# Kernel optimization log

Measured on AMD Instinct MI355X. Metric: run time of the kernel, lower is better.

The kernel has to match this reference:

```python
import jax, jax.numpy as jnp
import numpy as np

N, E, D = 50000, 512000, 128

def mish(x):
    return x * jnp.tanh(jax.nn.softplus(x))

def ln(x, g, b):
    m = jnp.mean(x, axis=-1, keepdims=True)
    v = jnp.var(x, axis=-1, keepdims=True)
    return (x - m) / jnp.sqrt(v + 1e-5) * g + b

def setup_inputs():
    key = jax.random.key(0)
    ks = jax.random.split(key, 16)
    W = lambda k, i, o: jax.random.normal(k, (i, o), jnp.float32) * 0.02
    z = jnp.zeros((D,), jnp.float32)
    o = jnp.ones((D,), jnp.float32)
    return {
        "node_feat": jax.random.normal(ks[0], (N, D), jnp.float32),
        "coord_feat": jax.random.normal(ks[1], (N, D), jnp.float32),
        "Wq": W(ks[2], D, D), "bq": z, "gq": o, "beq": z,
        "Wk": W(ks[3], D, D), "bk": z, "gk": o, "bek": z,
        "Wm1": W(ks[4], D, D), "bm1": z, "gm": o, "bem": z,
        "Wm2": W(ks[5], D, D), "bm2": z,
        "Wb1": W(ks[6], D, D), "bb1": z, "gb": o, "beb": z,
        "Wb2": W(ks[7], D, D), "bb2": z,
        "Ww1": W(ks[8], D, D), "bw1": z, "gw": o, "bew": z,
        "Ww2": W(ks[9], D, D), "bw2": z,
        "Wn1": W(ks[10], 2 * D, D), "bn1": z,
        "Wn2": W(ks[11], D, D), "bn2": z,
        "Wc1": W(ks[12], D, D), "bc1": z,
        "Wc2": W(ks[13], D, D),
        "src": jax.random.randint(ks[14], (E,), 0, N, jnp.int32),
        "dst": jax.random.randint(ks[15], (E,), 0, N, jnp.int32),
    }

def reference(node_feat, coord_feat, Wq, bq, gq, beq, Wk, bk, gk, bek,
              Wm1, bm1, gm, bem, Wm2, bm2, Wb1, bb1, gb, beb, Wb2, bb2,
              Ww1, bw1, gw, bew, Ww2, bw2, Wn1, bn1, Wn2, bn2, Wc1, bc1, Wc2,
              src, dst):
    # linear_q / linear_k on coord features: Linear -> LayerNorm -> Mish
    q = mish(ln(coord_feat @ Wq + bq, gq, beq))   # [N, D]
    k = mish(ln(coord_feat @ Wk + bk, gk, bek))   # [N, D]
    # u_sub_v('q','k'): per-edge q[src] - k[dst]
    rel = q[src] - k[dst]                          # [E, D]
    radial = jnp.sum(rel * rel, axis=-1, keepdims=True)  # [E, 1]
    rel = rel / jnp.sqrt(radial + 1e-8)
    # relative position encodings from dst coord features
    xd = coord_feat[dst]                           # [E, D]
    pem = mish(ln(xd @ Wm1 + bm1, gm, bem)) @ Wm2 + bm2
    peb = mish(ln(xd @ Wb1 + bb1, gb, beb)) @ Wb2 + bb2
    rel = rel * pem + peb
    # weight_encoding MLP
    w = mish(ln(rel @ Ww1 + bw1, gw, bew)) @ Ww2 + bw2  # [E, D]
    # dgl.softmax_edges over a single graph: softmax across the edge axis
    w = jax.nn.softmax(w, axis=0)
    # update_all(copy_e, sum): scatter-add edge weights to destination nodes
    h_neigh = jax.ops.segment_sum(w, dst, num_segments=N)  # [N, D]
    h = mish(jnp.concatenate([node_feat, h_neigh], axis=-1) @ Wn1 + bn1) @ Wn2 + bn2
    x = mish(coord_feat @ Wc1 + bc1) @ Wc2
    return (h, x)
```

## Files before the change

### kernel.cpp

```cpp
#include <hip/hip_runtime.h>
#include <cstdint>
#include <cstddef>

#define DN 128
#define NND 50000
#define NED 512000
#define NSCAN 49

typedef __attribute__((ext_vector_type(8))) short bf8;
typedef __attribute__((ext_vector_type(4))) float f4;
typedef unsigned short us;

__device__ __forceinline__ us f2bf(float f){
  union { float f; unsigned int u; } c; c.f = f;
  unsigned int r = c.u + 0x7fffu + ((c.u >> 16) & 1u);
  return (us)(r >> 16);
}
__device__ __forceinline__ float bf2f(us u){
  union { unsigned int u; float f; } c; c.u = ((unsigned int)u) << 16;
  return c.f;
}
__device__ __forceinline__ float mishf(float x){
  float e = __expf(x);
  float u = 1.f + e;
  float u2 = u * u;
  float t = (u2 - 1.f) / (u2 + 1.f);
  return x * ((x > 20.f) ? 1.f : t);
}

#define MFMA16(a, b, c) __builtin_amdgcn_mfma_f32_16x16x32_bf16((a), (b), (c), 0, 0, 0)

__device__ __forceinline__ bf8 lds_frag(const us* base, int row, int rowStrideB, int kElem){
  int byte = row * rowStrideB + kElem * 2;
  byte ^= (row & 7) << 4;
  return *(const bf8*)((const char*)base + byte);
}
__device__ __forceinline__ bf8 gfrag(const us* W, int n, int K, int kElem){
  return *(const bf8*)(W + (size_t)n * K + kElem);
}

template<int OUT_BF16>
__device__ __forceinline__ void store_tile(void* outp, int nrows, int r0,
                                           int wr, int wc, int g, int s, int ostride,
                                           const f4 (&A)[2][4]){
#pragma unroll
  for (int rt = 0; rt < 2; ++rt)
#pragma unroll
    for (int ct = 0; ct < 4; ++ct)
#pragma unroll
      for (int reg = 0; reg < 4; ++reg){
        int row = r0 + wr*32 + rt*16 + g*4 + reg;
        if (row < nrows){
          int col = wc*64 + ct*16 + s;
          float v = A[rt][ct][reg];
          if constexpr (OUT_BF16 != 0)
            ((us*)outp)[(size_t)row*ostride + col] = f2bf(v);
          else
            ((float*)outp)[(size_t)row*ostride + col] = v;
        }
      }
}

__device__ __forceinline__ void gemm_reg(const bf8 (&a)[2][4], const us* __restrict__ WT,
                                         const float* __restrict__ bias,
                                         int wc, int g, int s, f4 (&acc)[2][4]){
#pragma unroll
  for (int ct = 0; ct < 4; ++ct){
    float bv = bias ? bias[wc*64 + ct*16 + s] : 0.f;
    f4 t = {bv, bv, bv, bv};
    acc[0][ct] = t; acc[1][ct] = t;
  }
#pragma unroll
  for (int ct = 0; ct < 4; ++ct){
    int n = wc*64 + ct*16 + s;
#pragma unroll
    for (int kk = 0; kk < 4; ++kk){
      bf8 b = gfrag(WT, n, DN, kk*32 + g*8);
      acc[0][ct] = MFMA16(a[0][kk], b, acc[0][ct]);
      acc[1][ct] = MFMA16(a[1][kk], b, acc[1][ct]);
    }
  }
}

__device__ __forceinline__ void ln_mish(f4 (&acc)[2][4],
                                        const float* __restrict__ gam,
                                        const float* __restrict__ bet,
                                        int wr, int wc, int g, int s,
                                        float (*rowsum)[64][2], float (*rowsq)[64][2],
                                        int buf){
  float gv[4], bev[4];
#pragma unroll
  for (int ct = 0; ct < 4; ++ct){ int n = wc*64 + ct*16 + s; gv[ct] = gam[n]; bev[ct] = bet[n]; }
#pragma unroll
  for (int rt = 0; rt < 2; ++rt)
#pragma unroll
    for (int reg = 0; reg < 4; ++reg){
      float sm = acc[rt][0][reg] + acc[rt][1][reg] + acc[rt][2][reg] + acc[rt][3][reg];
      float sq = acc[rt][0][reg]*acc[rt][0][reg] + acc[rt][1][reg]*acc[rt][1][reg]
               + acc[rt][2][reg]*acc[rt][2][reg] + acc[rt][3][reg]*acc[rt][3][reg];
#pragma unroll
      for (int m = 1; m < 16; m <<= 1){ sm += __shfl_xor(sm, m, 64); sq += __shfl_xor(sq, m, 64); }
      if (s == 0){
        int row = wr*32 + rt*16 + g*4 + reg;
        rowsum[buf][row][wc] = sm; rowsq[buf][row][wc] = sq;
      }
    }
  __syncthreads();
#pragma unroll
  for (int rt = 0; rt < 2; ++rt)
#pragma unroll
    for (int reg = 0; reg < 4; ++reg){
      int row = wr*32 + rt*16 + g*4 + reg;
      float sm = rowsum[buf][row][0] + rowsum[buf][row][1];
      float sq = rowsq[buf][row][0] + rowsq[buf][row][1];
      float mu = sm * (1.f/128.f);
      float var = sq * (1.f/128.f) - mu*mu;
      float rs = rsqrtf(var + 1e-5f);
#pragma unroll
      for (int ct = 0; ct < 4; ++ct)
        acc[rt][ct][reg] = mishf((acc[rt][ct][reg] - mu) * rs * gv[ct] + bev[ct]);
    }
}

__device__ __forceinline__ void write_T(us* Tsh, int wr, int wc, int g, int s,
                                        const f4 (&A)[2][4]){
#pragma unroll
  for (int rt = 0; rt < 2; ++rt)
#pragma unroll
    for (int ct = 0; ct < 4; ++ct)
#pragma unroll
      for (int reg = 0; reg < 4; ++reg){
        int row = wr*32 + rt*16 + g*4 + reg;
        int col = wc*64 + ct*16 + s;
        int byte = row*256 + col*2; byte ^= (row & 7) << 4;
        *(us*)((char*)Tsh + byte) = f2bf(A[rt][ct][reg]);
      }
}

__device__ __forceinline__ void load_a2(const us* Tsh, int wr, int g, int s, bf8 (&a2)[2][4]){
#pragma unroll
  for (int rt = 0; rt < 2; ++rt)
#pragma unroll
    for (int kk = 0; kk < 4; ++kk)
      a2[rt][kk] = lds_frag(Tsh, wr*32 + rt*16 + s, 256, kk*32 + g*8);
}

__global__ __launch_bounds__(256, 2)
void node_fused(const float* __restrict__ X,
                const us* __restrict__ WqT,  const float* __restrict__ bq,
                const float* __restrict__ gq, const float* __restrict__ beq,
                const us* __restrict__ WkT,  const float* __restrict__ bk,
                const float* __restrict__ gk, const float* __restrict__ bek,
                const us* __restrict__ Wm1T, const float* __restrict__ bm1,
                const float* __restrict__ gm, const float* __restrict__ bem,
                const us* __restrict__ Wm2T, const float* __restrict__ bm2,
                const us* __restrict__ Wb1T, const float* __restrict__ bb1,
                const float* __restrict__ gb, const float* __restrict__ beb,
                const us* __restrict__ Wb2T, const float* __restrict__ bb2,
                const us* __restrict__ Wc1T, const float* __restrict__ bc1,
                const us* __restrict__ Wc2T,
                us* __restrict__ qt, us* __restrict__ kmb, float* __restrict__ xout)
{
  __shared__ us Ash[64 * DN];
  __shared__ float rowsum[2][64][2];
  __shared__ float rowsq[2][64][2];

  const int tid = threadIdx.x;
  const int r0 = blockIdx.x * 64;

  {
    int r = tid >> 2, c4 = tid & 3;
    int grow = r0 + r; if (grow >= NND) grow = NND - 1;
    const f4* sp = (const f4*)(X + (size_t)grow * DN + c4 * 32);
#pragma unroll
    for (int j = 0; j < 4; ++j){
      f4 v0 = sp[2*j], v1 = sp[2*j+1];
      bf8 o;
#pragma unroll
      for (int q = 0; q < 4; ++q){ o[q] = (short)f2bf(v0[q]); o[4+q] = (short)f2bf(v1[q]); }
      int byte = r*256 + c4*64 + j*16; byte ^= (r & 7) << 4;
      *(bf8*)((char*)Ash + byte) = o;
    }
  }
  __syncthreads();

  const int lane = tid & 63, w = tid >> 6;
  const int wr = w >> 1, wc = w & 1;
  const int g = lane >> 4, s = lane & 15;

  bf8 a[2][4];
#pragma unroll
  for (int rt = 0; rt < 2; ++rt)
#pragma unroll
    for (int kk = 0; kk < 4; ++kk)
      a[rt][kk] = lds_frag(Ash, wr*32 + rt*16 + s, 256, kk*32 + g*8);
  __syncthreads();

  f4 acc[2][4], acc2[2][4];
  bf8 a2[2][4];

  gemm_reg(a, WqT, bq, wc, g, s, acc);
  ln_mish(acc, gq, beq, wr, wc, g, s, rowsum, rowsq, 0);
  store_tile<1>((void*)qt, NND, r0, wr, wc, g, s, DN, acc);

  gemm_reg(a, WkT, bk, wc, g, s, acc);
  ln_mish(acc, gk, bek, wr, wc, g, s, rowsum, rowsq, 1);
  store_tile<1>((void*)kmb, NND, r0, wr, wc, g, s, 384, acc);

  gemm_reg(a, Wm1T, bm1, wc, g, s, acc);
  ln_mish(acc, gm, bem, wr, wc, g, s, rowsum, rowsq, 0);
  write_T(Ash, wr, wc, g, s, acc);
  __syncthreads();
  load_a2(Ash, wr, g, s, a2);
#pragma unroll
  for (int ct = 0; ct < 4; ++ct){
    float bv = bm2[wc*64 + ct*16 + s]; f4 t = {bv,bv,bv,bv}; acc2[0][ct] = t; acc2[1][ct] = t;
  }
#pragma unroll
  for (int ct = 0; ct < 4; ++ct){
    int n = wc*64 + ct*16 + s;
#pragma unroll
    for (int kk = 0; kk < 4; ++kk){
      bf8 b = gfrag(Wm2T, n, DN, kk*32 + g*8);
      acc2[0][ct] = MFMA16(a2[0][kk], b, acc2[0][ct]);
      acc2[1][ct] = MFMA16(a2[1][kk], b, acc2[1][ct]);
    }
  }
  store_tile<1>((void*)(kmb + 128), NND, r0, wr, wc, g, s, 384, acc2);

  gemm_reg(a, Wb1T, bb1, wc, g, s, acc);
  ln_mish(acc, gb, beb, wr, wc, g, s, rowsum, rowsq, 1);
  write_T(Ash, wr, wc, g, s, acc);
  __syncthreads();
  load_a2(Ash, wr, g, s, a2);
#pragma unroll
  for (int ct = 0; ct < 4; ++ct){
    float bv = bb2[wc*64 + ct*16 + s]; f4 t = {bv,bv,bv,bv}; acc2[0][ct] = t; acc2[1][ct] = t;
  }
#pragma unroll
  for (int ct = 0; ct < 4; ++ct){
    int n = wc*64 + ct*16 + s;
#pragma unroll
    for (int kk = 0; kk < 4; ++kk){
      bf8 b = gfrag(Wb2T, n, DN, kk*32 + g*8);
      acc2[0][ct] = MFMA16(a2[0][kk], b, acc2[0][ct]);
      acc2[1][ct] = MFMA16(a2[1][kk], b, acc2[1][ct]);
    }
  }
  store_tile<1>((void*)(kmb + 256), NND, r0, wr, wc, g, s, 384, acc2);

  gemm_reg(a, Wc1T, bc1, wc, g, s, acc);
#pragma unroll
  for (int rt = 0; rt < 2; ++rt)
#pragma unroll
    for (int ct = 0; ct < 4; ++ct)
#pragma unroll
      for (int reg = 0; reg < 4; ++reg)
        acc[rt][ct][reg] = mishf(acc[rt][ct][reg]);
  __syncthreads();
  write_T(Ash, wr, wc, g, s, acc);
  __syncthreads();
  load_a2(Ash, wr, g, s, a2);
#pragma unroll
  for (int ct = 0; ct < 4; ++ct){ f4 t = {0,0,0,0}; acc2[0][ct] = t; acc2[1][ct] = t; }
#pragma unroll
  for (int ct = 0; ct < 4; ++ct){
    int n = wc*64 + ct*16 + s;
#pragma unroll
    for (int kk = 0; kk < 4; ++kk){
      bf8 b = gfrag(Wc2T, n, DN, kk*32 + g*8);
      acc2[0][ct] = MFMA16(a2[0][kk], b, acc2[0][ct]);
      acc2[1][ct] = MFMA16(a2[1][kk], b, acc2[1][ct]);
    }
  }
  store_tile<0>((void*)xout, NND, r0, wr, wc, g, s, DN, acc2);
}

__global__ void csr_count(const int* __restrict__ dst, int* __restrict__ deg){
  int e = blockIdx.x * 256 + threadIdx.x;
  if (e < NED) atomicAdd(&deg[dst[e]], 1);
}

__global__ __launch_bounds__(1024) void csr_blocksum(const int* __restrict__ deg,
                                                     int* __restrict__ bsum){
  __shared__ int sb[1024];
  int t = threadIdx.x, idx = blockIdx.x * 1024 + t;
  sb[t] = (idx < NND) ? deg[idx] : 0;
  __syncthreads();
  for (int off = 512; off > 0; off >>= 1){
    if (t < off) sb[t] += sb[t + off];
    __syncthreads();
  }
  if (t == 0) bsum[blockIdx.x] = sb[0];
}

__global__ void csr_scanroot(const int* __restrict__ bsum, int* __restrict__ boff,
                             int* __restrict__ ptr){
  if (threadIdx.x == 0){
    int run = 0;
    for (int b = 0; b < NSCAN; ++b){ boff[b] = run; run += bsum[b]; }
    ptr[NND] = run;
  }
}

__global__ __launch_bounds__(1024) void csr_scatter(const int* __restrict__ deg,
                                                    const int* __restrict__ boff,
                                                    int* __restrict__ ptr,
                                                    int* __restrict__ fillctr){
  __shared__ int ss[1024];
  int t = threadIdx.x, idx = blockIdx.x * 1024 + t;
  int v = (idx < NND) ? deg[idx] : 0;
  ss[t] = v;
  __syncthreads();
  for (int off = 1; off < 1024; off <<= 1){
    int x = (t >= off) ? ss[t - off] : 0;
    __syncthreads();
    ss[t] += x;
    __syncthreads();
  }
  if (idx < NND){
    int p = boff[blockIdx.x] + ss[t] - v;
    ptr[idx] = p; fillctr[idx] = p;
  }
}

__global__ void csr_fill(const int* __restrict__ src, const int* __restrict__ dst,
                         int* __restrict__ fillctr,
                         int* __restrict__ ssorted, int* __restrict__ dsorted){
  int e = blockIdx.x * 256 + threadIdx.x;
  if (e < NED){
    int d = dst[e];
    int p = atomicAdd(&fillctr[d], 1);
    ssorted[p] = src[e];
    dsorted[p] = d;
  }
}

__global__ __launch_bounds__(256, 2)
void edge_kernel(const us* __restrict__ qtab,
                 const us* __restrict__ kmb,
                 const us* __restrict__ W1T,
                 const us* __restrict__ W2T,
                 const float* __restrict__ bw1,
                 const float* __restrict__ gwp,
                 const float* __restrict__ bewp,
                 const float* __restrict__ bw2,
                 const int* __restrict__ ssorted,
                 const int* __restrict__ dsorted,
                 us* __restrict__ pbuf,
                 float* __restrict__ colsum)
{
  __shared__ us Ash[64 * DN];
  __shared__ float rowsum[1][64][2];
  __shared__ float rowsq[1][64][2];
  __shared__ float csh[DN];

  const int tid = threadIdx.x;
  const int nchunk = gridDim.x >> 3;
  const int swz = (blockIdx.x & 7) * nchunk + (blockIdx.x >> 3);
  const int e0 = swz * 64;
  const int lane = tid & 63, w = tid >> 6;
  const int wr = w >> 1, wc = w & 1;
  const int g = lane >> 4, s = lane & 15;

  if (tid < DN) csh[tid] = 0.f;

  bf8 B1[4][4], B2[4][4];
  float b1v[4], gv[4], bev[4], b2v[4];
#pragma unroll
  for (int ct = 0; ct < 4; ++ct){
    int n = wc*64 + ct*16 + s;
#pragma unroll
    for (int kk = 0; kk < 4; ++kk){
      B1[ct][kk] = gfrag(W1T, n, DN, kk*32 + g*8);
      B2[ct][kk] = gfrag(W2T, n, DN, kk*32 + g*8);
    }
    b1v[ct] = bw1[n]; gv[ct] = gwp[n]; bev[ct] = bewp[n]; b2v[ct] = bw2[n];
  }

  {
    int r = tid >> 2, c4 = tid & 3;
    int e = e0 + r;
    int sn = ssorted[e], dn = dsorted[e];
    const bf8* qp = (const bf8*)(qtab + (size_t)sn * DN + c4 * 32);
    const us* kb = kmb + (size_t)dn * 384 + c4 * 32;
    float rel[32]; float ss = 0.f;
#pragma unroll
    for (int j = 0; j < 4; ++j){
      bf8 qv = qp[j];
      bf8 kv = *(const bf8*)(kb + j*8);
#pragma unroll
      for (int q = 0; q < 8; ++q){
        float d = bf2f((us)qv[q]) - bf2f((us)kv[q]);
        rel[j*8+q] = d; ss += d * d;
      }
    }
    ss += __shfl_xor(ss, 1, 64);
    ss += __shfl_xor(ss, 2, 64);
    float rinv = rsqrtf(ss + 1e-8f);
#pragma unroll
    for (int j = 0; j < 4; ++j){
      bf8 mv = *(const bf8*)(kb + 128 + j*8);
      bf8 bv = *(const bf8*)(kb + 256 + j*8);
      bf8 o;
#pragma unroll
      for (int q = 0; q < 8; ++q){
        float v = rel[j*8+q] * rinv * bf2f((us)mv[q]) + bf2f((us)bv[q]);
        o[q] = (short)f2bf(v);
      }
      int byte = r*256 + c4*64 + j*16; byte ^= (r & 7) << 4;
      *(bf8*)((char*)Ash + byte) = o;
    }
  }
  __syncthreads();

  f4 acc[2][4];
#pragma unroll
  for (int ct = 0; ct < 4; ++ct){ f4 t = {b1v[ct], b1v[ct], b1v[ct], b1v[ct]}; acc[0][ct] = t; acc[1][ct] = t; }
  bf8 a[2][4];
#pragma unroll
  for (int rt = 0; rt < 2; ++rt)
#pragma unroll
    for (int kk = 0; kk < 4; ++kk)
      a[rt][kk] = lds_frag(Ash, wr*32 + rt*16 + s, 256, kk*32 + g*8);
#pragma unroll
  for (int ct = 0; ct < 4; ++ct)
#pragma unroll
    for (int kk = 0; kk < 4; ++kk){
      acc[0][ct] = MFMA16(a[0][kk], B1[ct][kk], acc[0][ct]);
      acc[1][ct] = MFMA16(a[1][kk], B1[ct][kk], acc[1][ct]);
    }

#pragma unroll
  for (int rt = 0; rt < 2; ++rt)
#pragma unroll
    for (int reg = 0; reg < 4; ++reg){
      float sm = acc[rt][0][reg] + acc[rt][1][reg] + acc[rt][2][reg] + acc[rt][3][reg];
      float sq = acc[rt][0][reg]*acc[rt][0][reg] + acc[rt][1][reg]*acc[rt][1][reg]
               + acc[rt][2][reg]*acc[rt][2][reg] + acc[rt][3][reg]*acc[rt][3][reg];
#pragma unroll
      for (int m = 1; m < 16; m <<= 1){ sm += __shfl_xor(sm, m, 64); sq += __shfl_xor(sq, m, 64); }
      if (s == 0){
        int row = wr*32 + rt*16 + g*4 + reg;
        rowsum[0][row][wc] = sm; rowsq[0][row][wc] = sq;
      }
    }
  __syncthreads();
#pragma unroll
  for (int rt = 0; rt < 2; ++rt)
#pragma unroll
    for (int reg = 0; reg < 4; ++reg){
      int row = wr*32 + rt*16 + g*4 + reg;
      float sm = rowsum[0][row][0] + rowsum[0][row][1];
      float sq = rowsq[0][row][0] + rowsq[0][row][1];
      float mu = sm * (1.f/128.f);
      float var = sq * (1.f/128.f) - mu*mu;
      float rs = rsqrtf(var + 1e-5f);
#pragma unroll
      for (int ct = 0; ct < 4; ++ct)
        acc[rt][ct][reg] = mishf((acc[rt][ct][reg] - mu) * rs * gv[ct] + bev[ct]);
    }

  write_T(Ash, wr, wc, g, s, acc);
  __syncthreads();

  f4 p[2][4];
#pragma unroll
  for (int ct = 0; ct < 4; ++ct){ f4 t = {b2v[ct], b2v[ct], b2v[ct], b2v[ct]}; p[0][ct] = t; p[1][ct] = t; }
  bf8 a2[2][4];
  load_a2(Ash, wr, g, s, a2);
#pragma unroll
  for (int ct = 0; ct < 4; ++ct)
#pragma unroll
    for (int kk = 0; kk < 4; ++kk){
      p[0][ct] = MFMA16(a2[0][kk], B2[ct][kk], p[0][ct]);
      p[1][ct] = MFMA16(a2[1][kk], B2[ct][kk], p[1][ct]);
    }
#pragma unroll
  for (int rt = 0; rt < 2; ++rt)
#pragma unroll
    for (int ct = 0; ct < 4; ++ct)
#pragma unroll
      for (int reg = 0; reg < 4; ++reg)
        p[rt][ct][reg] = __expf(p[rt][ct][reg]);

#pragma unroll
  for (int ct = 0; ct < 4; ++ct){
    float cp = 0.f;
#pragma unroll
    for (int rt = 0; rt < 2; ++rt)
#pragma unroll
      for (int reg = 0; reg < 4; ++reg) cp += p[rt][ct][reg];
    cp += __shfl_xor(cp, 16, 64);
    cp += __shfl_xor(cp, 32, 64);
    if (g == 0) atomicAdd(&csh[wc*64 + ct*16 + s], cp);
  }
  __syncthreads();

  write_T(Ash, wr, wc, g, s, p);
  __syncthreads();

  {
    int r = tid >> 2, c4 = tid & 3;
    us* dp = pbuf + (size_t)(e0 + r) * DN + c4 * 32;
#pragma unroll
    for (int j = 0; j < 4; ++j){
      int byte = r*256 + c4*64 + j*16; byte ^= (r & 7) << 4;
      bf8 v = *(const bf8*)((const char*)Ash + byte);
      *(bf8*)(dp + j*8) = v;
    }
  }
  if (tid < DN) atomicAdd(&colsum[tid], csh[tid]);
}

__global__ __launch_bounds__(256, 2)
void final_h(const float* __restrict__ nodef,
             const us* __restrict__ pbuf,
             const int* __restrict__ ptr,
             const float* __restrict__ colsum,
             const us* __restrict__ Wn1T,
             const float* __restrict__ bn1,
             const us* __restrict__ Wn2T,
             const float* __restrict__ bn2,
             float* __restrict__ outh)
{
  __shared__ us Ash[64 * 256];

  const int tid = threadIdx.x;
  const int r0 = blockIdx.x * 64;
  const int lane = tid & 63, w = tid >> 6;

  {
    int r = tid >> 2, c4 = tid & 3;
    int grow = r0 + r; if (grow >= NND) grow = NND - 1;
    const f4* np = (const f4*)(nodef + (size_t)grow * DN + c4 * 32);
#pragma unroll
    for (int j = 0; j < 4; ++j){
      f4 v0 = np[2*j], v1 = np[2*j+1];
      bf8 o;
#pragma unroll
      for (int q = 0; q < 4; ++q){ o[q] = (short)f2bf(v0[q]); o[4+q] = (short)f2bf(v1[q]); }
      int byte = r*512 + c4*64 + j*16; byte ^= (r & 7) << 4;
      *(bf8*)((char*)Ash + byte) = o;
    }
  }

  {
    float c0 = colsum[lane*2], c1 = colsum[lane*2 + 1];
    for (int i = 0; i < 16; ++i){
      int lr = w*16 + i;
      int n = r0 + lr;
      float a0 = 0.f, a1 = 0.f;
      if (n < NND){
        int beg = ptr[n], end = ptr[n+1];
        for (int e = beg; e < end; ++e){
          unsigned int v = *(const unsigned int*)(pbuf + (size_t)e * DN + lane * 2);
          a0 += bf2f((us)(v & 0xffffu));
          a1 += bf2f((us)(v >> 16));
        }
      }
      unsigned int o = ((unsigned int)f2bf(a1 / c1) << 16) | (unsigned int)f2bf(a0 / c0);
      int byte = lr*512 + 256 + lane*4; byte ^= (lr & 7) << 4;
      *(unsigned int*)((char*)Ash + byte) = o;
    }
  }
  __syncthreads();

  const int wr = w >> 1, wc = w & 1;
  const int g = lane >> 4, s = lane & 15;

  float b1v[4], b2v[4];
#pragma unroll
  for (int ct = 0; ct < 4; ++ct){ int n = wc*64 + ct*16 + s; b1v[ct] = bn1[n]; b2v[ct] = bn2[n]; }

  f4 acc[2][4];
#pragma unroll
  for (int ct = 0; ct < 4; ++ct){ f4 t = {b1v[ct], b1v[ct], b1v[ct], b1v[ct]}; acc[0][ct] = t; acc[1][ct] = t; }

  bf8 a[2][8];
#pragma unroll
  for (int rt = 0; rt < 2; ++rt)
#pragma unroll
    for (int kk = 0; kk < 8; ++kk)
      a[rt][kk] = lds_frag(Ash, wr*32 + rt*16 + s, 512, kk*32 + g*8);
  __syncthreads();

#pragma unroll
  for (int ct = 0; ct < 4; ++ct){
    int n = wc*64 + ct*16 + s;
#pragma unroll
    for (int kk = 0; kk < 8; ++kk){
      bf8 b = gfrag(Wn1T, n, 256, kk*32 + g*8);
      acc[0][ct] = MFMA16(a[0][kk], b, acc[0][ct]);
      acc[1][ct] = MFMA16(a[1][kk], b, acc[1][ct]);
    }
  }

#pragma unroll
  for (int rt = 0; rt < 2; ++rt)
#pragma unroll
    for (int ct = 0; ct < 4; ++ct)
#pragma unroll
      for (int reg = 0; reg < 4; ++reg)
        acc[rt][ct][reg] = mishf(acc[rt][ct][reg]);
  write_T((us*)Ash, wr, wc, g, s, acc);
  __syncthreads();

  f4 acc2[2][4];
#pragma unroll
  for (int ct = 0; ct < 4; ++ct){ f4 t = {b2v[ct], b2v[ct], b2v[ct], b2v[ct]}; acc2[0][ct] = t; acc2[1][ct] = t; }
  bf8 a2[2][4];
  load_a2((const us*)Ash, wr, g, s, a2);
#pragma unroll
  for (int ct = 0; ct < 4; ++ct){
    int n = wc*64 + ct*16 + s;
#pragma unroll
    for (int kk = 0; kk < 4; ++kk){
      bf8 b = gfrag(Wn2T, n, DN, kk*32 + g*8);
      acc2[0][ct] = MFMA16(a2[0][kk], b, acc2[0][ct]);
      acc2[1][ct] = MFMA16(a2[1][kk], b, acc2[1][ct]);
    }
  }
  store_tile<0>((void*)outh, NND, r0, wr, wc, g, s, DN, acc2);
}

struct WPrepArgs {
  const float* w[12];
  us* wt[12];
  int K[12];
};

__global__ void prep_weights(WPrepArgs a){
  int widx = blockIdx.y;
  int K = a.K[widx];
  int idx = blockIdx.x * 256 + threadIdx.x;
  if (idx >= DN * K) return;
  int kshift = (K == 256) ? 8 : 7;
  int n = idx >> kshift;
  int k = idx & (K - 1);
  a.wt[widx][idx] = f2bf(a.w[widx][(size_t)k * DN + n]);
}

extern "C" void kernel_launch(void* const* d_in, const int* in_sizes, int n_in,
                              void* d_out, int out_size, void* d_ws, size_t ws_size,
                              hipStream_t stream) {
  const float* node_feat = (const float*)d_in[0];
  const float* coordf    = (const float*)d_in[1];
  const float* Wq  = (const float*)d_in[2];
  const float* bq  = (const float*)d_in[3];
  const float* gq  = (const float*)d_in[4];
  const float* beq = (const float*)d_in[5];
  const float* Wk  = (const float*)d_in[6];
  const float* bk  = (const float*)d_in[7];
  const float* gk  = (const float*)d_in[8];
  const float* bek = (const float*)d_in[9];
  const float* Wm1 = (const float*)d_in[10];
  const float* bm1 = (const float*)d_in[11];
  const float* gm  = (const float*)d_in[12];
  const float* bem = (const float*)d_in[13];
  const float* Wm2 = (const float*)d_in[14];
  const float* bm2 = (const float*)d_in[15];
  const float* Wb1 = (const float*)d_in[16];
  const float* bb1 = (const float*)d_in[17];
  const float* gb  = (const float*)d_in[18];
  const float* beb = (const float*)d_in[19];
  const float* Wb2 = (const float*)d_in[20];
  const float* bb2 = (const float*)d_in[21];
  const float* Ww1 = (const float*)d_in[22];
  const float* bw1 = (const float*)d_in[23];
  const float* gw  = (const float*)d_in[24];
  const float* bew = (const float*)d_in[25];
  const float* Ww2 = (const float*)d_in[26];
  const float* bw2 = (const float*)d_in[27];
  const float* Wn1 = (const float*)d_in[28];
  const float* bn1 = (const float*)d_in[29];
  const float* Wn2 = (const float*)d_in[30];
  const float* bn2 = (const float*)d_in[31];
  const float* Wc1 = (const float*)d_in[32];
  const float* bc1 = (const float*)d_in[33];
  const float* Wc2 = (const float*)d_in[34];
  const int* srcI  = (const int*)d_in[35];
  const int* dstI  = (const int*)d_in[36];

  char* ws = (char*)d_ws;
  size_t off = 0;
  auto alloc = [&](size_t bytes) -> char* {
    char* p = ws + off;
    off += (bytes + 255) & ~(size_t)255;
    return p;
  };
  us*    qt      = (us*)alloc((size_t)NND * DN * 2);
  us*    kmb     = (us*)alloc((size_t)NND * 384 * 2);
  us*    pbuf    = (us*)alloc((size_t)NED * DN * 2);
  float* colsum  = (float*)alloc(DN * 4);
  int*   deg     = (int*)alloc((size_t)NND * 4);
  int*   ptr     = (int*)alloc((size_t)(NND + 1) * 4);
  int*   fillctr = (int*)alloc((size_t)NND * 4);
  int*   ssorted = (int*)alloc((size_t)NED * 4);
  int*   dsorted = (int*)alloc((size_t)NED * 4);
  int*   bsum    = (int*)alloc((size_t)NSCAN * 4);
  int*   boff    = (int*)alloc((size_t)NSCAN * 4);
  us*    wtb     = (us*)alloc((size_t)12 * 16384 * 2);

  hipMemsetAsync(colsum, 0, DN * 4, stream);
  hipMemsetAsync(deg, 0, (size_t)NND * 4, stream);

  WPrepArgs pa;
  const float* wsrc[12] = {Wq, Wk, Wm1, Wm2, Wb1, Wb2, Ww1, Ww2, Wc1, Wc2, Wn2, Wn1};
  for (int i = 0; i < 12; ++i){
    pa.w[i] = wsrc[i];
    pa.wt[i] = wtb + (size_t)i * 16384;
    pa.K[i] = (i == 11) ? 256 : 128;
  }
  prep_weights<<<dim3(128, 12), 256, 0, stream>>>(pa);

  csr_count<<<(NED + 255) / 256, 256, 0, stream>>>(dstI, deg);
  csr_blocksum<<<NSCAN, 1024, 0, stream>>>(deg, bsum);
  csr_scanroot<<<1, 64, 0, stream>>>(bsum, boff, ptr);
  csr_scatter<<<NSCAN, 1024, 0, stream>>>(deg, boff, ptr, fillctr);
  csr_fill<<<(NED + 255) / 256, 256, 0, stream>>>(srcI, dstI, fillctr, ssorted, dsorted);

  const int NB = (NND + 63) / 64;

  node_fused<<<NB, 256, 0, stream>>>(coordf,
      pa.wt[0], bq, gq, beq,
      pa.wt[1], bk, gk, bek,
      pa.wt[2], bm1, gm, bem, pa.wt[3], bm2,
      pa.wt[4], bb1, gb, beb, pa.wt[5], bb2,
      pa.wt[8], bc1, pa.wt[9],
      qt, kmb, (float*)d_out + (size_t)NND * DN);

  edge_kernel<<<NED / 64, 256, 0, stream>>>(qt, kmb, pa.wt[6], pa.wt[7],
                                            bw1, gw, bew, bw2, ssorted, dsorted, pbuf, colsum);

  final_h<<<NB, 256, 0, stream>>>(node_feat, pbuf, ptr, colsum,
                                  pa.wt[11], bn1, pa.wt[10], bn2, (float*)d_out);
}
```

Before: 601.3 us.

## Segment-reduce edge weights into per-node accumulator with atomics instead of edge buffer

The edge kernel no longer writes a per-edge bf16 buffer that final_h later re-reads through CSR pointers. Each block instead run-length reduces its dst-sorted rows in LDS and atomically adds partial sums into a float per-node accumulator. Column sums are spread over 8 replicated slots to reduce atomic contention. This drops the large edge-sized write plus gather read, at the cost of a 25.6MB memset and float atomic traffic on global memory.

After: 517.1 us. 1.16x faster.

```diff
diff --git a/kernel.cpp b/kernel.cpp
--- a/kernel.cpp
+++ b/kernel.cpp
@@ -294,18 +294,15 @@
   if (t == 0) bsum[blockIdx.x] = sb[0];
 }
 
-__global__ void csr_scanroot(const int* __restrict__ bsum, int* __restrict__ boff,
-                             int* __restrict__ ptr){
+__global__ void csr_scanroot(const int* __restrict__ bsum, int* __restrict__ boff){
   if (threadIdx.x == 0){
     int run = 0;
     for (int b = 0; b < NSCAN; ++b){ boff[b] = run; run += bsum[b]; }
-    ptr[NND] = run;
   }
 }
 
 __global__ __launch_bounds__(1024) void csr_scatter(const int* __restrict__ deg,
                                                     const int* __restrict__ boff,
-                                                    int* __restrict__ ptr,
                                                     int* __restrict__ fillctr){
   __shared__ int ss[1024];
   int t = threadIdx.x, idx = blockIdx.x * 1024 + t;
@@ -320,7 +317,7 @@
   }
   if (idx < NND){
     int p = boff[blockIdx.x] + ss[t] - v;
-    ptr[idx] = p; fillctr[idx] = p;
+    fillctr[idx] = p;
   }
 }
 
@@ -347,13 +344,13 @@
                  const float* __restrict__ bw2,
                  const int* __restrict__ ssorted,
                  const int* __restrict__ dsorted,
-                 us* __restrict__ pbuf,
-                 float* __restrict__ colsum)
+                 float* __restrict__ hacc,
+                 float* __restrict__ colsum8)
 {
   __shared__ us Ash[64 * DN];
   __shared__ float rowsum[1][64][2];
   __shared__ float rowsq[1][64][2];
-  __shared__ float csh[DN];
+  __shared__ int dsh[64];
 
   const int tid = threadIdx.x;
   const int nchunk = gridDim.x >> 3;
@@ -363,7 +360,7 @@
   const int wr = w >> 1, wc = w & 1;
   const int g = lane >> 4, s = lane & 15;
 
-  if (tid < DN) csh[tid] = 0.f;
+  if (tid < 64) dsh[tid] = dsorted[e0 + tid];
 
   bf8 B1[4][4], B2[4][4];
   float b1v[4], gv[4], bev[4], b2v[4];
@@ -484,40 +481,39 @@
       for (int reg = 0; reg < 4; ++reg)
         p[rt][ct][reg] = __expf(p[rt][ct][reg]);
 
-#pragma unroll
-  for (int ct = 0; ct < 4; ++ct){
-    float cp = 0.f;
-#pragma unroll
-    for (int rt = 0; rt < 2; ++rt)
-#pragma unroll
-      for (int reg = 0; reg < 4; ++reg) cp += p[rt][ct][reg];
-    cp += __shfl_xor(cp, 16, 64);
-    cp += __shfl_xor(cp, 32, 64);
-    if (g == 0) atomicAdd(&csh[wc*64 + ct*16 + s], cp);
-  }
   __syncthreads();
 
   write_T(Ash, wr, wc, g, s, p);
   __syncthreads();
 
   {
-    int r = tid >> 2, c4 = tid & 3;
-    us* dp = pbuf + (size_t)(e0 + r) * DN + c4 * 32;
-#pragma unroll
-    for (int j = 0; j < 4; ++j){
-      int byte = r*256 + c4*64 + j*16; byte ^= (r & 7) << 4;
-      bf8 v = *(const bf8*)((const char*)Ash + byte);
-      *(bf8*)(dp + j*8) = v;
-    }
-  }
-  if (tid < DN) atomicAdd(&colsum[tid], csh[tid]);
+    int col = tid & 127, half = tid >> 7;
+    int rbeg = half * 32;
+    float csum = 0.f;
+    int prev = dsh[rbeg];
+    float run = 0.f;
+#pragma unroll 8
+    for (int r = rbeg; r < rbeg + 32; ++r){
+      int d = dsh[r];
+      int byte = r*256 + col*2; byte ^= (r & 7) << 4;
+      float v = bf2f(*(const us*)((const char*)Ash + byte));
+      csum += v;
+      if (d != prev){
+        atomicAdd(&hacc[(size_t)prev * DN + col], run);
+        run = v; prev = d;
+      } else {
+        run += v;
+      }
+    }
+    atomicAdd(&hacc[(size_t)prev * DN + col], run);
+    atomicAdd(&colsum8[(blockIdx.x & 7) * DN + col], csum);
+  }
 }
 
 __global__ __launch_bounds__(256, 2)
 void final_h(const float* __restrict__ nodef,
-             const us* __restrict__ pbuf,
-             const int* __restrict__ ptr,
-             const float* __restrict__ colsum,
+             const float* __restrict__ hacc,
+             const float* __restrict__ colsum8,
              const us* __restrict__ Wn1T,
              const float* __restrict__ bn1,
              const us* __restrict__ Wn2T,
@@ -525,15 +521,24 @@
              float* __restrict__ outh)
 {
   __shared__ us Ash[64 * 256];
+  __shared__ float rcs[DN];
 
   const int tid = threadIdx.x;
   const int r0 = blockIdx.x * 64;
-  const int lane = tid & 63, w = tid >> 6;
+
+  if (tid < DN){
+    float ssum = 0.f;
+#pragma unroll
+    for (int x = 0; x < 8; ++x) ssum += colsum8[x * DN + tid];
+    rcs[tid] = 1.f / ssum;
+  }
+  __syncthreads();
 
   {
     int r = tid >> 2, c4 = tid & 3;
     int grow = r0 + r; if (grow >= NND) grow = NND - 1;
     const f4* np = (const f4*)(nodef + (size_t)grow * DN + c4 * 32);
+    const f4* hp = (const f4*)(hacc + (size_t)grow * DN + c4 * 32);
 #pragma unroll
     for (int j = 0; j < 4; ++j){
       f4 v0 = np[2*j], v1 = np[2*j+1];
@@ -542,30 +547,20 @@
       for (int q = 0; q < 4; ++q){ o[q] = (short)f2bf(v0[q]); o[4+q] = (short)f2bf(v1[q]); }
       int byte = r*512 + c4*64 + j*16; byte ^= (r & 7) << 4;
       *(bf8*)((char*)Ash + byte) = o;
-    }
-  }
-
-  {
-    float c0 = colsum[lane*2], c1 = colsum[lane*2 + 1];
-    for (int i = 0; i < 16; ++i){
-      int lr = w*16 + i;
-      int n = r0 + lr;
-      float a0 = 0.f, a1 = 0.f;
-      if (n < NND){
-        int beg = ptr[n], end = ptr[n+1];
-        for (int e = beg; e < end; ++e){
-          unsigned int v = *(const unsigned int*)(pbuf + (size_t)e * DN + lane * 2);
-          a0 += bf2f((us)(v & 0xffffu));
-          a1 += bf2f((us)(v >> 16));
-        }
+      f4 h0 = hp[2*j], h1 = hp[2*j+1];
+      bf8 o2;
+#pragma unroll
+      for (int q = 0; q < 4; ++q){
+        o2[q]   = (short)f2bf(h0[q] * rcs[c4*32 + j*8 + q]);
+        o2[4+q] = (short)f2bf(h1[q] * rcs[c4*32 + j*8 + 4 + q]);
       }
-      unsigned int o = ((unsigned int)f2bf(a1 / c1) << 16) | (unsigned int)f2bf(a0 / c0);
-      int byte = lr*512 + 256 + lane*4; byte ^= (lr & 7) << 4;
-      *(unsigned int*)((char*)Ash + byte) = o;
-    }
-  }
-  __syncthreads();
-
+      int byte2 = r*512 + 256 + c4*64 + j*16; byte2 ^= (r & 7) << 4;
+      *(bf8*)((char*)Ash + byte2) = o2;
+    }
+  }
+  __syncthreads();
+
+  const int lane = tid & 63, w = tid >> 6;
   const int wr = w >> 1, wc = w & 1;
   const int g = lane >> 4, s = lane & 15;
 
@@ -691,10 +686,9 @@
   };
   us*    qt      = (us*)alloc((size_t)NND * DN * 2);
   us*    kmb     = (us*)alloc((size_t)NND * 384 * 2);
-  us*    pbuf    = (us*)alloc((size_t)NED * DN * 2);
-  float* colsum  = (float*)alloc(DN * 4);
+  float* hacc    = (float*)alloc((size_t)NND * DN * 4);
+  float* colsum8 = (float*)alloc(8 * DN * 4);
   int*   deg     = (int*)alloc((size_t)NND * 4);
-  int*   ptr     = (int*)alloc((size_t)(NND + 1) * 4);
   int*   fillctr = (int*)alloc((size_t)NND * 4);
   int*   ssorted = (int*)alloc((size_t)NED * 4);
   int*   dsorted = (int*)alloc((size_t)NED * 4);
@@ -702,7 +696,7 @@
   int*   boff    = (int*)alloc((size_t)NSCAN * 4);
   us*    wtb     = (us*)alloc((size_t)12 * 16384 * 2);
 
-  hipMemsetAsync(colsum, 0, DN * 4, stream);
+  hipMemsetAsync(hacc, 0, (size_t)NND * DN * 4 + 8 * DN * 4, stream);
   hipMemsetAsync(deg, 0, (size_t)NND * 4, stream);
 
   WPrepArgs pa;
@@ -716,8 +710,8 @@
 
   csr_count<<<(NED + 255) / 256, 256, 0, stream>>>(dstI, deg);
   csr_blocksum<<<NSCAN, 1024, 0, stream>>>(deg, bsum);
-  csr_scanroot<<<1, 64, 0, stream>>>(bsum, boff, ptr);
-  csr_scatter<<<NSCAN, 1024, 0, stream>>>(deg, boff, ptr, fillctr);
+  csr_scanroot<<<1, 64, 0, stream>>>(bsum, boff);
+  csr_scatter<<<NSCAN, 1024, 0, stream>>>(deg, boff, fillctr);
   csr_fill<<<(NED + 255) / 256, 256, 0, stream>>>(srcI, dstI, fillctr, ssorted, dsorted);
 
   const int NB = (NND + 63) / 64;
@@ -731,8 +725,9 @@
       qt, kmb, (float*)d_out + (size_t)NND * DN);
 
   edge_kernel<<<NED / 64, 256, 0, stream>>>(qt, kmb, pa.wt[6], pa.wt[7],
-                                            bw1, gw, bew, bw2, ssorted, dsorted, pbuf, colsum);
-
-  final_h<<<NB, 256, 0, stream>>>(node_feat, pbuf, ptr, colsum,
+                                            bw1, gw, bew, bw2, ssorted, dsorted,
+                                            hacc, colsum8);
+
+  final_h<<<NB, 256, 0, stream>>>(node_feat, hacc, colsum8,
                                   pa.wt[11], bn1, pa.wt[10], bn2, (float*)d_out);
 }
```
